# Kernel optimization log

Hardware: AMD Instinct MI355X
Metric: run time of the kernel (lower is better)

Reference implementation:

```python
import jax, jax.numpy as jnp
import numpy as np

MAX_DEPTH = 11  # node positions < 2**11 = 2048


def setup_inputs() -> dict:
    key = jax.random.key(0)
    k1, k2, k3, k4, k5 = jax.random.split(key, 5)
    B, S, dim = 4, 1024, 64
    token_types = jax.random.randint(k1, (B, S), 0, 5).astype(jnp.int32)
    # token_values in [-1, 2]: -1 marks out-of-scope for scope tokens;
    # bop uses tv+1 (0..3), nop uses tv+5 (4..7) -- all in-range for the 11-row table
    token_values = (jax.random.randint(k2, (B, S), 0, 4) - 1).astype(jnp.int32)
    node_positions = jax.random.randint(k3, (B, S), 0, 2048).astype(jnp.int32)
    embed_table = jax.random.normal(k4, (11, dim), dtype=jnp.float32)
    # mirrors torch.rand(2,dim,dim).softmax(-1).cumsum(-1) init
    primitives_raw = jnp.cumsum(
        jax.nn.softmax(jax.random.uniform(k5, (2, dim, dim), dtype=jnp.float32), axis=-1),
        axis=-1)
    return {
        "token_types": token_types,
        "token_values": token_values,
        "node_positions": node_positions,
        "embed_table": embed_table,
        "primitives_raw": primitives_raw,
    }


def _forward(token_types, token_values, node_positions, embed_table, primitives_raw):
    dim = embed_table.shape[1]
    B, S = token_types.shape

    # primitives = expm(P - P^H) for each of the 2 generators
    herm = primitives_raw - jnp.swapaxes(primitives_raw, -1, -2)
    prims = jax.vmap(jax.scipy.linalg.expm)(herm)  # [2, dim, dim]

    # --- positional encodings via binary-path matrix products ---
    # path(pos) applies prims[pos%2], then prims[(pos//2)%2], ... until pos==1.
    # Equivalent to the original's per-unique-position masked-linear loop,
    # evaluated per token (== positional_encodings[inverse]).
    maps = jnp.broadcast_to(jnp.eye(dim, dtype=embed_table.dtype), (B, S, dim, dim))
    pos = node_positions
    for _ in range(MAX_DEPTH):
        active = pos > 1
        bit = (pos & 1).astype(jnp.int32)
        step_p = prims[bit]  # [B, S, dim, dim] gather of the per-step generator
        # linear(maps, prim) == maps @ prim.T, applied rowwise to each map matrix
        stepped = jnp.einsum('bsij,bskj->bsik', maps, step_p)
        maps = jnp.where(active[..., None, None], stepped, maps)
        pos = pos >> 1

    # --- content embeddings via masked gathers ---
    tt, tv = token_types, token_values
    sos = tt == 0
    bop = tt == 1
    nop = tt == 2
    scope = tt == 3
    oos = scope & (tv == -1)
    db = tt == 4
    idx = jnp.where(sos, 0,
          jnp.where(bop, tv + 1,
          jnp.where(nop, tv + 5,
          jnp.where(db, 8,
          jnp.where(oos, 10, 0)))))
    valid = sos | bop | nop | db | oos  # in-scope scope tokens stay zero
    content = jnp.where(valid[..., None], embed_table[idx], jnp.zeros((), embed_table.dtype))
    return content, maps


def reference(token_types, token_values, node_positions, embed_table, primitives_raw):
    return _forward(token_types, token_values, node_positions, embed_table, primitives_raw)
```

## Files before the change

kernel.cpp:

```cpp
#include <hip/hip_runtime.h>
#include <hip/hip_bf16.h>
#include <stdint.h>

typedef __attribute__((ext_vector_type(4))) float fx4;
typedef __attribute__((ext_vector_type(16))) float fx16;
typedef __attribute__((ext_vector_type(8))) short bx8;
typedef unsigned short u16;
typedef unsigned int u32;

#define LDW 72
#define PL (64 * LDW)
#define MAGIC 0x9E3779B9u


__device__ __forceinline__ u16 f2bf(float x) {
    u32 u = __float_as_uint(x);
    return (u16)((u + 0x7FFFu + ((u >> 16) & 1u)) >> 16);
}
__device__ __forceinline__ float bf2f(u16 h) { return __uint_as_float(((u32)h) << 16); }

__device__ __forceinline__ bx8 ld32(const u16* p, int band, int kc, int l) {
    return *(const bx8*)(p + (band * 32 + (l & 31)) * LDW + kc * 16 + (l >> 5) * 8);
}

__device__ __forceinline__ void mmG1(const u16* z1h, const u16* z1l,
                                     const u16* z2h, const u16* z2l,
                                     int ti, int tj, int l, fx16& acc) {
    fx16 ca, cb, cc;
#pragma unroll
    for (int i = 0; i < 16; ++i) { ca[i] = 0.f; cb[i] = 0.f; cc[i] = 0.f; }
#pragma unroll
    for (int kc = 0; kc < 4; ++kc) {
        bx8 ah = ld32(z1h, ti, kc, l), al = ld32(z1l, ti, kc, l);
        bx8 bh = ld32(z2h, tj, kc, l), bl = ld32(z2l, tj, kc, l);
        ca = __builtin_amdgcn_mfma_f32_32x32x16_bf16(ah, bh, ca, 0, 0, 0);
        cb = __builtin_amdgcn_mfma_f32_32x32x16_bf16(ah, bl, cb, 0, 0, 0);
        cc = __builtin_amdgcn_mfma_f32_32x32x16_bf16(al, bh, cc, 0, 0, 0);
    }
#pragma unroll
    for (int i = 0; i < 16; ++i) acc[i] = ca[i] + (cb[i] + cc[i]);
}

__device__ __forceinline__ void mmG2(const u16* z1h, const u16* z1l,
                                     const u16* z2h, const u16* z2l,
                                     int ti, int tj, int l, fx16& acc) {
    fx16 ca, cb, cc;
#pragma unroll
    for (int i = 0; i < 16; ++i) { ca[i] = 0.f; cb[i] = 0.f; cc[i] = 0.f; }
#pragma unroll
    for (int kc = 0; kc < 4; ++kc) {
        bx8 ah = ld32(z1h, ti, kc, l), al = ld32(z1l, ti, kc, l);
        bx8 bh = ld32(z2h, tj, kc, l), bl = ld32(z2l, tj, kc, l);
        ca = __builtin_amdgcn_mfma_f32_32x32x16_bf16(bh, ah, ca, 0, 0, 0);
        cb = __builtin_amdgcn_mfma_f32_32x32x16_bf16(bh, al, cb, 0, 0, 0);
        cc = __builtin_amdgcn_mfma_f32_32x32x16_bf16(bl, ah, cc, 0, 0, 0);
    }
#pragma unroll
    for (int i = 0; i < 16; ++i) acc[i] = ca[i] + (cb[i] + cc[i]);
}

__device__ __forceinline__ void stP(u16* hi, u16* lo, int TI, int TJ, int l, const fx16& a) {
    const int Ar = TJ * 32 + (l & 31);
    const int c0 = TI * 32 + 4 * (l >> 5);
#pragma unroll
    for (int q = 0; q < 4; ++q) {
        union { u16 u[4]; uint2 v; } H, L;
#pragma unroll
        for (int r = 0; r < 4; ++r) {
            float v = a[4 * q + r];
            u32 u = __float_as_uint(v);
            H.u[r] = (u16)(u >> 16);
            L.u[r] = f2bf(v - __uint_as_float(u & 0xFFFF0000u));
        }
        *(uint2*)(hi + Ar * LDW + c0 + q * 8) = H.v;
        *(uint2*)(lo + Ar * LDW + c0 + q * 8) = L.v;
    }
}

__device__ __forceinline__ void stG(u16* T, int TI, int TJ, int l, const fx16& a) {
    const int Ar = TJ * 32 + (l & 31);
    const int c0 = TI * 32 + 4 * (l >> 5);
#pragma unroll
    for (int q = 0; q < 4; ++q) {
        union { u16 u[4]; uint2 v; } pk;
#pragma unroll
        for (int r = 0; r < 4; ++r) pk.u[r] = f2bf(a[4 * q + r]);
        *(uint2*)(T + Ar * 64 + c0 + q * 8) = pk.v;
    }
}

__device__ __forceinline__ void epiT32(fx16& a, const float* Mf,
                                       int TI, int TJ, int l, float qa, float qb) {
    const int gc = TJ * 32 + (l & 31);
    const int r0 = TI * 32 + 4 * (l >> 5);
#pragma unroll
    for (int q = 0; q < 4; ++q)
#pragma unroll
        for (int r = 0; r < 4; ++r) {
            const int gr = r0 + q * 8 + r;
            float m = Mf[gc * 65 + gr];
            a[4 * q + r] += qb * m + (gr == gc ? qa : 0.f);
        }
}
__device__ __forceinline__ void epiN32(fx16& a, const float* Mf,
                                       int TI, int TJ, int l, float qa, float qb) {
    const int gc = TJ * 32 + (l & 31);
    const int r0 = TI * 32 + 4 * (l >> 5);
#pragma unroll
    for (int q = 0; q < 4; ++q)
#pragma unroll
        for (int r = 0; r < 4; ++r) {
            const int gr = r0 + q * 8 + r;
            float m = Mf[gr * 65 + gc];
            a[4 * q + r] += qb * m + (gr == gc ? qa : 0.f);
        }
}

__global__ __launch_bounds__(512) void tables_kernel(const float* __restrict__ praw,
                                                     u16* __restrict__ wsP,
                                                     u16* __restrict__ rm_bf,
                                                     u16* __restrict__ cm_bf,
                                                     u32* __restrict__ flags)
{
    __shared__ u16 S[14 * PL];
    __shared__ float Mf[64 * 65];
    const int p = blockIdx.x, tid = threadIdx.x;
    const int w = tid >> 6, l = tid & 63;
    const int wid = w & 3, half = w >> 2;
    const int ti = wid & 1, tj = wid >> 1;

    if (p < 2) {
        const int g = p;
        const float* P = praw + g * 4096;
        u16* p0h = S;            u16* p0l = S + PL;
        u16* p1h = S + 2 * PL;   u16* p1l = S + 3 * PL;
        u16* p2h = S + 4 * PL;   u16* p2l = S + 5 * PL;
        u16* p3h = S + 6 * PL;   u16* p3l = S + 7 * PL;

        for (int s = tid; s < 4096; s += 512) {
            const int r = s >> 6, c = s & 63;
            const float m = (P[r * 64 + c] - P[c * 64 + r]) * 0.0625f;
            Mf[r * 65 + c] = m;
            u32 um = __float_as_uint(m);
            float lof = m - __uint_as_float(um & 0xFFFF0000u);
            u16 hh = (u16)(um >> 16), ll = f2bf(lof);
            p0h[r * LDW + c] = hh;  p0l[r * LDW + c] = ll;
            p1h[c * LDW + r] = hh;  p1l[c * LDW + r] = ll;
        }
        __syncthreads();

        fx16 acc;

        if (half == 0) {
            mmG1(p1h, p1l, p0h, p0l, ti, tj, l, acc);
            stP(p2h, p2l, ti, tj, l, acc);
        } else {
            const float C8 = 2.48015873015873e-5f, C9 = 2.75573192239859e-6f;
            for (int s = tid - 256; s < 4096; s += 256) {
                const int r = s >> 6, c = s & 63;
                float v = C9 * Mf[r * 65 + c] + (r == c ? C8 : 0.f);
                u32 u = __float_as_uint(v);
                p3h[r * LDW + c] = (u16)(u >> 16);
                p3l[r * LDW + c] = f2bf(v - __uint_as_float(u & 0xFFFF0000u));
            }
        }
        __syncthreads();

        if (half == 0) {
            mmG1(p2h, p2l, p3h, p3l, ti, tj, l, acc);
            epiT32(acc, Mf, ti, tj, l, 1.388888888888889e-3f, 1.984126984126984e-4f);
            stP(p0h, p0l, ti, tj, l, acc);
        }
        __syncthreads();
        if (half == 0) {
            mmG1(p2h, p2l, p0h, p0l, ti, tj, l, acc);
            epiT32(acc, Mf, ti, tj, l, 4.166666666666667e-2f, 8.333333333333333e-3f);
            stP(p3h, p3l, ti, tj, l, acc);
        }
        __syncthreads();
        if (half == 0) {
            mmG1(p2h, p2l, p3h, p3l, ti, tj, l, acc);
            epiT32(acc, Mf, ti, tj, l, 0.5f, 1.666666666666667e-1f);
            stP(p0h, p0l, ti, tj, l, acc);
        }
        __syncthreads();
        if (half == 0) {
            mmG1(p2h, p2l, p0h, p0l, ti, tj, l, acc);
            epiT32(acc, Mf, ti, tj, l, 1.f, 1.f);
            stP(p3h, p3l, ti, tj, l, acc);
        } else {
            mmG2(p2h, p2l, p0h, p0l, ti, tj, l, acc);
            epiN32(acc, Mf, tj, ti, l, 1.f, 1.f);
            stP(p1h, p1l, tj, ti, l, acc);
        }
        __syncthreads();

        u16 *Ych = p1h, *Ycl = p1l, *Xch = p3h, *Xcl = p3l;
        u16 *Ynh = p2h, *Ynl = p2l, *Xnh = p0h, *Xnl = p0l;
#pragma unroll 1
        for (int s4 = 0; s4 < 4; ++s4) {
            if (half == 0) {
                mmG1(Ych, Ycl, Xch, Xcl, ti, tj, l, acc);
                stP(Xnh, Xnl, ti, tj, l, acc);
            } else {
                mmG2(Ych, Ycl, Xch, Xcl, ti, tj, l, acc);
                stP(Ynh, Ynl, tj, ti, l, acc);
            }
            __syncthreads();
            u16* t;
            t = Xch; Xch = Xnh; Xnh = t;   t = Xcl; Xcl = Xnl; Xnl = t;
            t = Ych; Ych = Ynh; Ynh = t;   t = Ycl; Ycl = Ynl; Ynl = t;
        }

        {
            const int base = tid * 8, r = base >> 6, c = base & 63;
            u16* dst = wsP + g * 16384;
            *(uint4*)(dst + base)         = *(const uint4*)(Ych + r * LDW + c);
            *(uint4*)(dst + 4096 + base)  = *(const uint4*)(Ycl + r * LDW + c);
            *(uint4*)(dst + 8192 + base)  = *(const uint4*)(Xch + r * LDW + c);
            *(uint4*)(dst + 12288 + base) = *(const uint4*)(Xcl + r * LDW + c);
        }
        __threadfence();
        __syncthreads();
        if (tid < 64) atomicExch(&flags[(g * 64 + tid) * 32], MAGIC);

        for (int s = tid; s < 4096; s += 512) {
            u16 v = ((s >> 6) == (s & 63)) ? (u16)0x3F80 : (u16)0;
            rm_bf[p * 4096 + s] = v;
            cm_bf[p * 4096 + s] = v;
        }
        return;
    }

    if (tid == 0) {
        while (atomicOr(&flags[(0 * 64 + p) * 32], 0u) != MAGIC) __builtin_amdgcn_s_sleep(8);
        while (atomicOr(&flags[(1 * 64 + p) * 32], 0u) != MAGIC) __builtin_amdgcn_s_sleep(8);
    }
    __syncthreads();
    __threadfence();

    const int d = 31 - __clz(p);

    if (d == 1) {
        const u16* src = wsP + (p & 1) * 16384;
        for (int s = tid; s < 4096; s += 512) {
            rm_bf[p * 4096 + s] = f2bf(bf2f(src[s]) + bf2f(src[4096 + s]));
            cm_bf[p * 4096 + s] = f2bf(bf2f(src[8192 + s]) + bf2f(src[12288 + s]));
        }
        return;
    }

    {
        const int base = tid * 8, r = base >> 6, c = base & 63;
        const int off = r * LDW + c;
        *(uint4*)(S + 0 * PL + off) = *(const uint4*)(wsP + base);
        *(uint4*)(S + 1 * PL + off) = *(const uint4*)(wsP + 4096 + base);
        *(uint4*)(S + 2 * PL + off) = *(const uint4*)(wsP + 8192 + base);
        *(uint4*)(S + 3 * PL + off) = *(const uint4*)(wsP + 12288 + base);
        *(uint4*)(S + 4 * PL + off) = *(const uint4*)(wsP + 16384 + base);
        *(uint4*)(S + 5 * PL + off) = *(const uint4*)(wsP + 16384 + 4096 + base);
        *(uint4*)(S + 6 * PL + off) = *(const uint4*)(wsP + 16384 + 8192 + base);
        *(uint4*)(S + 7 * PL + off) = *(const uint4*)(wsP + 16384 + 12288 + base);
    }
    __syncthreads();

    const int b0 = p & 1, b1 = (p >> 1) & 1, b2 = (p >> 2) & 1, b3 = (p >> 3) & 1,
              b4 = (p >> 4) & 1;
    const u16 *rm0h = S + b0 * 4 * PL,          *rm0l = rm0h + PL;
    const u16 *cm1h = S + b1 * 4 * PL + 2 * PL, *cm1l = cm1h + PL;
    const u16 *rm2h = S + b2 * 4 * PL,          *rm2l = rm2h + PL;
    const u16 *cm3h = S + b3 * 4 * PL + 2 * PL, *cm3l = cm3h + PL;
    u16 *PAh = S + 8 * PL,  *PAl = S + 9 * PL;
    u16 *PBh = S + 10 * PL, *PBl = S + 11 * PL;
    u16 *PCh = S + 12 * PL, *PCl = S + 13 * PL;

    fx16 acc;
    const u16 *fz1h, *fz1l, *fz2h, *fz2l;

    if (d == 2) {
        fz1h = cm1h; fz1l = cm1l; fz2h = rm0h; fz2l = rm0l;
    } else if (d == 3) {
        if (half == 0) {
            mmG1(cm1h, cm1l, rm0h, rm0l, ti, tj, l, acc);
            stP(PAh, PAl, ti, tj, l, acc);
        }
        __syncthreads();
        const u16* c2h = S + b2 * 4 * PL + 2 * PL;
        fz1h = c2h; fz1l = c2h + PL; fz2h = PAh; fz2l = PAl;
    } else {
        if (half == 0) {
            mmG1(cm1h, cm1l, rm0h, rm0l, ti, tj, l, acc);
            stP(PAh, PAl, ti, tj, l, acc);
        } else {
            mmG2(cm3h, cm3l, rm2h, rm2l, ti, tj, l, acc);
            stP(PBh, PBl, tj, ti, l, acc);
        }
        __syncthreads();
        if (d == 4) {
            fz1h = PBh; fz1l = PBl; fz2h = PAh; fz2l = PAl;
        } else {
            if (half == 0) {
                mmG1(PBh, PBl, PAh, PAl, ti, tj, l, acc);
                stP(PCh, PCl, ti, tj, l, acc);
            }
            __syncthreads();
            const u16* c4h = S + b4 * 4 * PL + 2 * PL;
            fz1h = c4h; fz1l = c4h + PL; fz2h = PCh; fz2l = PCl;
        }
    }

    if (half == 0) {
        mmG1(fz1h, fz1l, fz2h, fz2l, ti, tj, l, acc);
        stG(rm_bf + p * 4096, ti, tj, l, acc);
    } else {
        mmG2(fz1h, fz1l, fz2h, fz2l, ti, tj, l, acc);
        stG(cm_bf + p * 4096, tj, ti, l, acc);
    }
}

__global__ __launch_bounds__(256) void out_kernel(const int* __restrict__ tt,
                                                  const int* __restrict__ tv,
                                                  const int* __restrict__ npos,
                                                  const float* __restrict__ embed,
                                                  const u16* __restrict__ rm_bf,
                                                  const u16* __restrict__ cm_bf,
                                                  float* __restrict__ out)
{
    __shared__ float ST[4][16 * 64];
    const int tid = threadIdx.x;
    const int wv = tid >> 6, l = tid & 63;
    const int flat = blockIdx.x * 4 + wv;
    const int pos = npos[flat];

    {
        const int t = tt[flat], v = tv[flat];
        int idx; bool valid = true;
        if (t == 0)      idx = 0;
        else if (t == 1) idx = v + 1;
        else if (t == 2) idx = v + 5;
        else if (t == 4) idx = 8;
        else if (t == 3 && v == -1) idx = 10;
        else { idx = 0; valid = false; }
        out[flat * 64 + l] = valid ? embed[idx * 64 + l] : 0.f;
    }

    float* om = out + 4096 * 64 + (size_t)flat * 4096;

    if (pos < 64) {
        const u16* src = rm_bf + pos * 4096;
#pragma unroll
        for (int i = 0; i < 16; ++i) {
            const int f0 = i * 256 + l * 4;
            uint2 ld = *(const uint2*)(src + f0);
            fx4 v;
            v[0] = __uint_as_float(ld.x << 16); v[1] = __uint_as_float(ld.x & 0xFFFF0000u);
            v[2] = __uint_as_float(ld.y << 16); v[3] = __uint_as_float(ld.y & 0xFFFF0000u);
            *(fx4*)(om + f0) = v;
        }
    } else {
        const int lo5 = (pos & 31) | 32;
        const int hi5 = pos >> 5;
        const u16* Acm = cm_bf + hi5 * 4096;
        const u16* Brm = rm_bf + lo5 * 4096;
        const int lr = l & 15, h = l >> 4, k8 = h * 8;
        float* st = ST[wv];

        bx8 A0[4], A1[4], B0[4], B1[4];
#pragma unroll
        for (int q = 0; q < 4; ++q) {
            A0[q] = *(const bx8*)(Acm + (q * 16 + lr) * 64 + k8);
            A1[q] = *(const bx8*)(Acm + (q * 16 + lr) * 64 + 32 + k8);
        }
#pragma unroll
        for (int c = 0; c < 4; ++c) {
            B0[c] = *(const bx8*)(Brm + (c * 16 + lr) * 64 + k8);
            B1[c] = *(const bx8*)(Brm + (c * 16 + lr) * 64 + 32 + k8);
        }
#pragma unroll
        for (int ct = 0; ct < 4; ++ct) {
#pragma unroll
            for (int q = 0; q < 4; ++q) {
                fx4 c4 = { 0.f, 0.f, 0.f, 0.f };
                c4 = __builtin_amdgcn_mfma_f32_16x16x32_bf16(A0[q], B0[ct], c4, 0, 0, 0);
                c4 = __builtin_amdgcn_mfma_f32_16x16x32_bf16(A1[q], B1[ct], c4, 0, 0, 0);
                *(fx4*)(st + lr * 64 + 4 * ((4 * q + h) ^ lr)) = c4;
            }
#pragma unroll
            for (int i2 = 0; i2 < 4; ++i2) {
                const int row = i2 * 4 + h;
                fx4 v = *(const fx4*)(st + row * 64 + 4 * ((l & 15) ^ row));
                *(fx4*)(om + ct * 1024 + i2 * 256 + l * 4) = v;
            }
        }
    }
}

extern "C" void kernel_launch(void* const* d_in, const int* in_sizes, int n_in,
                              void* d_out, int out_size, void* d_ws, size_t ws_size,
                              hipStream_t stream)
{
    const int*   tt    = (const int*)d_in[0];
    const int*   tv    = (const int*)d_in[1];
    const int*   np    = (const int*)d_in[2];
    const float* embed = (const float*)d_in[3];
    const float* praw  = (const float*)d_in[4];
    float* out = (float*)d_out;

    u32* flags = (u32*)d_ws;
    u16* wsP   = (u16*)((char*)d_ws + 16384);
    u16* rm_bf = (u16*)((char*)d_ws + 16384 + 65536);
    u16* cm_bf = (u16*)((char*)d_ws + 16384 + 65536 + 524288);

    tables_kernel<<<dim3(64), dim3(512), 0, stream>>>(praw, wsP, rm_bf, cm_bf, flags);
    out_kernel<<<dim3(1024), dim3(256), 0, stream>>>(tt, tv, np, embed, rm_bf, cm_bf, out);
}
```

Measured before the change: 38.38 us.

## Split expm matrix products into 16x16 MFMA tiles across all eight waves

The expm table kernel's 64x64 split-bf16 products move from 32x32 MFMA tiles computed by only four waves (the other half idle during the Horner steps) to 16x16x32 MFMA tiles. Each of the eight waves handles two or four tiles, so every wave has work in each serial step. This shortens the critical path of the dependent Horner chain and squaring loop, at the cost of more LDS fragment loads per FLOP and smaller MFMA shapes.

```diff
diff --git a/kernel.cpp b/kernel.cpp
--- a/kernel.cpp
+++ b/kernel.cpp
@@ -89,31 +89,64 @@
     }
 }
 
-__device__ __forceinline__ void epiT32(fx16& a, const float* Mf,
+__device__ __forceinline__ fx4 core16(const u16* z1h, const u16* z1l,
+                                      const u16* z2h, const u16* z2l,
+                                      int TI, int TJ, int l) {
+    const int lr = l & 15, k8 = (l >> 4) * 8;
+    const u16* pa = z1h + (TI * 16 + lr) * LDW + k8;
+    const u16* pal = z1l + (TI * 16 + lr) * LDW + k8;
+    const u16* pb = z2h + (TJ * 16 + lr) * LDW + k8;
+    const u16* pbl = z2l + (TJ * 16 + lr) * LDW + k8;
+    bx8 a0h = *(const bx8*)(pa),       a0l = *(const bx8*)(pal);
+    bx8 a1h = *(const bx8*)(pa + 32),  a1l = *(const bx8*)(pal + 32);
+    bx8 b0h = *(const bx8*)(pb),       b0l = *(const bx8*)(pbl);
+    bx8 b1h = *(const bx8*)(pb + 32),  b1l = *(const bx8*)(pbl + 32);
+    fx4 chh = {0.f,0.f,0.f,0.f}, chl = {0.f,0.f,0.f,0.f}, clh = {0.f,0.f,0.f,0.f};
+    chh = __builtin_amdgcn_mfma_f32_16x16x32_bf16(a0h, b0h, chh, 0, 0, 0);
+    chl = __builtin_amdgcn_mfma_f32_16x16x32_bf16(a0h, b0l, chl, 0, 0, 0);
+    clh = __builtin_amdgcn_mfma_f32_16x16x32_bf16(a0l, b0h, clh, 0, 0, 0);
+    chh = __builtin_amdgcn_mfma_f32_16x16x32_bf16(a1h, b1h, chh, 0, 0, 0);
+    chl = __builtin_amdgcn_mfma_f32_16x16x32_bf16(a1h, b1l, chl, 0, 0, 0);
+    clh = __builtin_amdgcn_mfma_f32_16x16x32_bf16(a1l, b1h, clh, 0, 0, 0);
+    fx4 r;
+#pragma unroll
+    for (int i = 0; i < 4; ++i) r[i] = chh[i] + (chl[i] + clh[i]);
+    return r;
+}
+
+__device__ __forceinline__ void stP16(u16* hi, u16* lo, int TI, int TJ, int l, fx4 a) {
+    const int Ar = TJ * 16 + (l & 15);
+    const int Ac = TI * 16 + 4 * (l >> 4);
+    union { u16 u[4]; uint2 v; } H, L;
+#pragma unroll
+    for (int r = 0; r < 4; ++r) {
+        u32 u = __float_as_uint(a[r]);
+        H.u[r] = (u16)(u >> 16);
+        L.u[r] = f2bf(a[r] - __uint_as_float(u & 0xFFFF0000u));
+    }
+    *(uint2*)(hi + Ar * LDW + Ac) = H.v;
+    *(uint2*)(lo + Ar * LDW + Ac) = L.v;
+}
+
+__device__ __forceinline__ void epiT16(fx4& a, const float* Mf,
                                        int TI, int TJ, int l, float qa, float qb) {
-    const int gc = TJ * 32 + (l & 31);
-    const int r0 = TI * 32 + 4 * (l >> 5);
-#pragma unroll
-    for (int q = 0; q < 4; ++q)
-#pragma unroll
-        for (int r = 0; r < 4; ++r) {
-            const int gr = r0 + q * 8 + r;
-            float m = Mf[gc * 65 + gr];
-            a[4 * q + r] += qb * m + (gr == gc ? qa : 0.f);
-        }
-}
-__device__ __forceinline__ void epiN32(fx16& a, const float* Mf,
+    const int gc = TJ * 16 + (l & 15);
+    const int r0 = TI * 16 + 4 * (l >> 4);
+#pragma unroll
+    for (int r = 0; r < 4; ++r) {
+        const int gr = r0 + r;
+        a[r] += qb * Mf[gc * 65 + gr] + (gr == gc ? qa : 0.f);
+    }
+}
+__device__ __forceinline__ void epiN16(fx4& a, const float* Mf,
                                        int TI, int TJ, int l, float qa, float qb) {
-    const int gc = TJ * 32 + (l & 31);
-    const int r0 = TI * 32 + 4 * (l >> 5);
-#pragma unroll
-    for (int q = 0; q < 4; ++q)
-#pragma unroll
-        for (int r = 0; r < 4; ++r) {
-            const int gr = r0 + q * 8 + r;
-            float m = Mf[gr * 65 + gc];
-            a[4 * q + r] += qb * m + (gr == gc ? qa : 0.f);
-        }
+    const int gc = TJ * 16 + (l & 15);
+    const int r0 = TI * 16 + 4 * (l >> 4);
+#pragma unroll
+    for (int r = 0; r < 4; ++r) {
+        const int gr = r0 + r;
+        a[r] += qb * Mf[gr * 65 + gc] + (gr == gc ? qa : 0.f);
+    }
 }
 
 __global__ __launch_bounds__(512) void tables_kernel(const float* __restrict__ praw,
@@ -149,14 +182,17 @@
         }
         __syncthreads();
 
-        fx16 acc;
-
-        if (half == 0) {
-            mmG1(p1h, p1l, p0h, p0l, ti, tj, l, acc);
-            stP(p2h, p2l, ti, tj, l, acc);
-        } else {
+        fx4 a;
+
+#pragma unroll
+        for (int q = 0; q < 2; ++q) {
+            const int t = w * 2 + q, TI = t >> 2, TJ = t & 3;
+            a = core16(p1h, p1l, p0h, p0l, TI, TJ, l);
+            stP16(p2h, p2l, TI, TJ, l, a);
+        }
+        {
             const float C8 = 2.48015873015873e-5f, C9 = 2.75573192239859e-6f;
-            for (int s = tid - 256; s < 4096; s += 256) {
+            for (int s = tid; s < 4096; s += 512) {
                 const int r = s >> 6, c = s & 63;
                 float v = C9 * Mf[r * 65 + c] + (r == c ? C8 : 0.f);
                 u32 u = __float_as_uint(v);
@@ -166,32 +202,42 @@
         }
         __syncthreads();
 
-        if (half == 0) {
-            mmG1(p2h, p2l, p3h, p3l, ti, tj, l, acc);
-            epiT32(acc, Mf, ti, tj, l, 1.388888888888889e-3f, 1.984126984126984e-4f);
-            stP(p0h, p0l, ti, tj, l, acc);
-        }
-        __syncthreads();
-        if (half == 0) {
-            mmG1(p2h, p2l, p0h, p0l, ti, tj, l, acc);
-            epiT32(acc, Mf, ti, tj, l, 4.166666666666667e-2f, 8.333333333333333e-3f);
-            stP(p3h, p3l, ti, tj, l, acc);
-        }
-        __syncthreads();
-        if (half == 0) {
-            mmG1(p2h, p2l, p3h, p3l, ti, tj, l, acc);
-            epiT32(acc, Mf, ti, tj, l, 0.5f, 1.666666666666667e-1f);
-            stP(p0h, p0l, ti, tj, l, acc);
-        }
-        __syncthreads();
-        if (half == 0) {
-            mmG1(p2h, p2l, p0h, p0l, ti, tj, l, acc);
-            epiT32(acc, Mf, ti, tj, l, 1.f, 1.f);
-            stP(p3h, p3l, ti, tj, l, acc);
-        } else {
-            mmG2(p2h, p2l, p0h, p0l, ti, tj, l, acc);
-            epiN32(acc, Mf, tj, ti, l, 1.f, 1.f);
-            stP(p1h, p1l, tj, ti, l, acc);
+#pragma unroll
+        for (int q = 0; q < 2; ++q) {
+            const int t = w * 2 + q, TI = t >> 2, TJ = t & 3;
+            a = core16(p2h, p2l, p3h, p3l, TI, TJ, l);
+            epiT16(a, Mf, TI, TJ, l, 1.388888888888889e-3f, 1.984126984126984e-4f);
+            stP16(p0h, p0l, TI, TJ, l, a);
+        }
+        __syncthreads();
+#pragma unroll
+        for (int q = 0; q < 2; ++q) {
+            const int t = w * 2 + q, TI = t >> 2, TJ = t & 3;
+            a = core16(p2h, p2l, p0h, p0l, TI, TJ, l);
+            epiT16(a, Mf, TI, TJ, l, 4.166666666666667e-2f, 8.333333333333333e-3f);
+            stP16(p3h, p3l, TI, TJ, l, a);
+        }
+        __syncthreads();
+#pragma unroll
+        for (int q = 0; q < 2; ++q) {
+            const int t = w * 2 + q, TI = t >> 2, TJ = t & 3;
+            a = core16(p2h, p2l, p3h, p3l, TI, TJ, l);
+            epiT16(a, Mf, TI, TJ, l, 0.5f, 1.666666666666667e-1f);
+            stP16(p0h, p0l, TI, TJ, l, a);
+        }
+        __syncthreads();
+#pragma unroll
+        for (int q = 0; q < 4; ++q) {
+            const int u = w * 4 + q, v = u & 15, TI = v >> 2, TJ = v & 3;
+            if (u < 16) {
+                a = core16(p2h, p2l, p0h, p0l, TI, TJ, l);
+                epiT16(a, Mf, TI, TJ, l, 1.f, 1.f);
+                stP16(p3h, p3l, TI, TJ, l, a);
+            } else {
+                a = core16(p0h, p0l, p2h, p2l, TI, TJ, l);
+                epiN16(a, Mf, TI, TJ, l, 1.f, 1.f);
+                stP16(p1h, p1l, TI, TJ, l, a);
+            }
         }
         __syncthreads();
 
@@ -199,12 +245,16 @@
         u16 *Ynh = p2h, *Ynl = p2l, *Xnh = p0h, *Xnl = p0l;
 #pragma unroll 1
         for (int s4 = 0; s4 < 4; ++s4) {
-            if (half == 0) {
-                mmG1(Ych, Ycl, Xch, Xcl, ti, tj, l, acc);
-                stP(Xnh, Xnl, ti, tj, l, acc);
-            } else {
-                mmG2(Ych, Ycl, Xch, Xcl, ti, tj, l, acc);
-                stP(Ynh, Ynl, tj, ti, l, acc);
+#pragma unroll
+            for (int q = 0; q < 4; ++q) {
+                const int u = w * 4 + q, v = u & 15, TI = v >> 2, TJ = v & 3;
+                if (u < 16) {
+                    a = core16(Ych, Ycl, Xch, Xcl, TI, TJ, l);
+                    stP16(Xnh, Xnl, TI, TJ, l, a);
+                } else {
+                    a = core16(Xch, Xcl, Ych, Ycl, TI, TJ, l);
+                    stP16(Ynh, Ynl, TI, TJ, l, a);
+                }
             }
             __syncthreads();
             u16* t;
```

Result: slower. 39.86 us (+3.9%).

## Restructure matrix exponential Taylor evaluation using odd/even split with cubed generator

Applied to the files above, without the earlier changes.

The degree-9 Taylor polynomial for expm is re-evaluated by exploiting antisymmetry. M^2 and M^3 are computed and stored, then a Paterson–Stockmeyer-style Horner in M^3 builds the polynomial. The exp(-M) term (the transpose) comes from the same intermediate products instead of a separate mmG2 transposed multiply. This aims to cut the serial chain of small matmuls and barriers in the expm prologue. It adds an extra fp32 scratch buffer in shared memory and leaves one half of the block idle for most stages.

```diff
diff --git a/kernel.cpp b/kernel.cpp
--- a/kernel.cpp
+++ b/kernel.cpp
@@ -87,33 +87,6 @@
         for (int r = 0; r < 4; ++r) pk.u[r] = f2bf(a[4 * q + r]);
         *(uint2*)(T + Ar * 64 + c0 + q * 8) = pk.v;
     }
-}
-
-__device__ __forceinline__ void epiT32(fx16& a, const float* Mf,
-                                       int TI, int TJ, int l, float qa, float qb) {
-    const int gc = TJ * 32 + (l & 31);
-    const int r0 = TI * 32 + 4 * (l >> 5);
-#pragma unroll
-    for (int q = 0; q < 4; ++q)
-#pragma unroll
-        for (int r = 0; r < 4; ++r) {
-            const int gr = r0 + q * 8 + r;
-            float m = Mf[gc * 65 + gr];
-            a[4 * q + r] += qb * m + (gr == gc ? qa : 0.f);
-        }
-}
-__device__ __forceinline__ void epiN32(fx16& a, const float* Mf,
-                                       int TI, int TJ, int l, float qa, float qb) {
-    const int gc = TJ * 32 + (l & 31);
-    const int r0 = TI * 32 + 4 * (l >> 5);
-#pragma unroll
-    for (int q = 0; q < 4; ++q)
-#pragma unroll
-        for (int r = 0; r < 4; ++r) {
-            const int gr = r0 + q * 8 + r;
-            float m = Mf[gr * 65 + gc];
-            a[4 * q + r] += qb * m + (gr == gc ? qa : 0.f);
-        }
 }
 
 __global__ __launch_bounds__(512) void tables_kernel(const float* __restrict__ praw,
@@ -136,6 +109,13 @@
         u16* p1h = S + 2 * PL;   u16* p1l = S + 3 * PL;
         u16* p2h = S + 4 * PL;   u16* p2l = S + 5 * PL;
         u16* p3h = S + 6 * PL;   u16* p3l = S + 7 * PL;
+        float* Mf2 = (float*)(S + 8 * PL);
+
+        const float c0c = 1.0f, c1c = 1.0f, c2c = 0.5f;
+        const float c3c = 1.666666666666667e-1f, c4c = 4.166666666666667e-2f;
+        const float c5c = 8.333333333333333e-3f, c6c = 1.388888888888889e-3f;
+        const float c7c = 1.984126984126984e-4f, c8c = 2.48015873015873e-5f;
+        const float c9c = 2.75573192239859e-6f;
 
         for (int s = tid; s < 4096; s += 512) {
             const int r = s >> 6, c = s & 63;
@@ -149,54 +129,77 @@
         }
         __syncthreads();
 
-        fx16 acc;
+        fx16 acc, v;
+        const int gcb = tj * 32 + (l & 31);
+        const int r0b = ti * 32 + 4 * (l >> 5);
 
         if (half == 0) {
             mmG1(p1h, p1l, p0h, p0l, ti, tj, l, acc);
             stP(p2h, p2l, ti, tj, l, acc);
+#pragma unroll
+            for (int q = 0; q < 4; ++q)
+#pragma unroll
+                for (int rr = 0; rr < 4; ++rr)
+                    Mf2[(r0b + q * 8 + rr) * 65 + gcb] = acc[4 * q + rr];
+        }
+        __syncthreads();
+
+        if (half == 0) {
+            mmG1(p2h, p2l, p0h, p0l, ti, tj, l, acc);
+            stP(p3h, p3l, ti, tj, l, acc);
+#pragma unroll
+            for (int q = 0; q < 4; ++q)
+#pragma unroll
+                for (int rr = 0; rr < 4; ++rr) {
+                    const int gr = r0b + q * 8 + rr;
+                    v[4 * q + rr] = c9c * acc[4 * q + rr] + c8c * Mf2[gr * 65 + gcb]
+                                  - c7c * Mf[gr * 65 + gcb] + (gr == gcb ? c6c : 0.f);
+                }
+            stP(p1h, p1l, ti, tj, l, v);
+        }
+        __syncthreads();
+
+        if (half == 0) {
+            mmG1(p3h, p3l, p1h, p1l, ti, tj, l, acc);
+#pragma unroll
+            for (int q = 0; q < 4; ++q)
+#pragma unroll
+                for (int rr = 0; rr < 4; ++rr) {
+                    const int gr = r0b + q * 8 + rr;
+                    v[4 * q + rr] = -acc[4 * q + rr] + c5c * Mf2[gr * 65 + gcb]
+                                  - c4c * Mf[gr * 65 + gcb] + (gr == gcb ? c3c : 0.f);
+                }
+            stP(p0h, p0l, ti, tj, l, v);
+        }
+        __syncthreads();
+
+        if (half == 0) {
+            mmG1(p3h, p3l, p0h, p0l, ti, tj, l, acc);
+#pragma unroll
+            for (int q = 0; q < 4; ++q)
+#pragma unroll
+                for (int rr = 0; rr < 4; ++rr) {
+                    const int gr = r0b + q * 8 + rr;
+                    v[4 * q + rr] = -acc[4 * q + rr] + c2c * Mf2[gr * 65 + gcb]
+                                  - c1c * Mf[gr * 65 + gcb] + (gr == gcb ? c0c : 0.f);
+                }
+            stP(p1h, p1l, ti, tj, l, v);
         } else {
-            const float C8 = 2.48015873015873e-5f, C9 = 2.75573192239859e-6f;
-            for (int s = tid - 256; s < 4096; s += 256) {
-                const int r = s >> 6, c = s & 63;
-                float v = C9 * Mf[r * 65 + c] + (r == c ? C8 : 0.f);
-                u32 u = __float_as_uint(v);
-                p3h[r * LDW + c] = (u16)(u >> 16);
-                p3l[r * LDW + c] = f2bf(v - __uint_as_float(u & 0xFFFF0000u));
-            }
-        }
-        __syncthreads();
-
-        if (half == 0) {
-            mmG1(p2h, p2l, p3h, p3l, ti, tj, l, acc);
-            epiT32(acc, Mf, ti, tj, l, 1.388888888888889e-3f, 1.984126984126984e-4f);
-            stP(p0h, p0l, ti, tj, l, acc);
-        }
-        __syncthreads();
-        if (half == 0) {
-            mmG1(p2h, p2l, p0h, p0l, ti, tj, l, acc);
-            epiT32(acc, Mf, ti, tj, l, 4.166666666666667e-2f, 8.333333333333333e-3f);
-            stP(p3h, p3l, ti, tj, l, acc);
-        }
-        __syncthreads();
-        if (half == 0) {
-            mmG1(p2h, p2l, p3h, p3l, ti, tj, l, acc);
-            epiT32(acc, Mf, ti, tj, l, 0.5f, 1.666666666666667e-1f);
-            stP(p0h, p0l, ti, tj, l, acc);
-        }
-        __syncthreads();
-        if (half == 0) {
-            mmG1(p2h, p2l, p0h, p0l, ti, tj, l, acc);
-            epiT32(acc, Mf, ti, tj, l, 1.f, 1.f);
-            stP(p3h, p3l, ti, tj, l, acc);
-        } else {
-            mmG2(p2h, p2l, p0h, p0l, ti, tj, l, acc);
-            epiN32(acc, Mf, tj, ti, l, 1.f, 1.f);
-            stP(p1h, p1l, tj, ti, l, acc);
-        }
-        __syncthreads();
-
-        u16 *Ych = p1h, *Ycl = p1l, *Xch = p3h, *Xcl = p3l;
-        u16 *Ynh = p2h, *Ynl = p2l, *Xnh = p0h, *Xnl = p0l;
+            mmG1(p0h, p0l, p3h, p3l, ti, tj, l, acc);
+#pragma unroll
+            for (int q = 0; q < 4; ++q)
+#pragma unroll
+                for (int rr = 0; rr < 4; ++rr) {
+                    const int gr = r0b + q * 8 + rr;
+                    v[4 * q + rr] = -acc[4 * q + rr] + c2c * Mf2[gr * 65 + gcb]
+                                  + c1c * Mf[gr * 65 + gcb] + (gr == gcb ? c0c : 0.f);
+                }
+            stP(p2h, p2l, ti, tj, l, v);
+        }
+        __syncthreads();
+
+        u16 *Ych = p2h, *Ycl = p2l, *Xch = p1h, *Xcl = p1l;
+        u16 *Ynh = p3h, *Ynl = p3l, *Xnh = p0h, *Xnl = p0l;
 #pragma unroll 1
         for (int s4 = 0; s4 < 4; ++s4) {
             if (half == 0) {
@@ -225,9 +228,9 @@
         if (tid < 64) atomicExch(&flags[(g * 64 + tid) * 32], MAGIC);
 
         for (int s = tid; s < 4096; s += 512) {
-            u16 v = ((s >> 6) == (s & 63)) ? (u16)0x3F80 : (u16)0;
-            rm_bf[p * 4096 + s] = v;
-            cm_bf[p * 4096 + s] = v;
+            u16 vv = ((s >> 6) == (s & 63)) ? (u16)0x3F80 : (u16)0;
+            rm_bf[p * 4096 + s] = vv;
+            cm_bf[p * 4096 + s] = vv;
         }
         return;
     }
```

Result: faster. 37.23 us, median of 2 (-3.0%).
